# Optimization experiments

Measured on AMD Instinct MI355X. Metric: run time of the kernel, lower is better.

The kernel has to match this reference:

```python
import jax, jax.numpy as jnp
import numpy as np

B, C, H, W = 8, 128, 48, 48
RED = 16  # SELayer reduction


def setup_inputs() -> dict:
    key = jax.random.key(0)
    ks = jax.random.split(key, 8)
    s = 0.05  # weight scale for numerical stability of softmax
    return {
        "x": jax.random.normal(ks[0], (B, C, H, W), jnp.float32),
        "Wq": jax.random.normal(ks[1], (C, C), jnp.float32) * s,
        "bq": jnp.zeros((C,), jnp.float32),
        "Wk": jax.random.normal(ks[2], (C, C), jnp.float32) * s,
        "bk": jnp.zeros((C,), jnp.float32),
        "Wv": jax.random.normal(ks[3], (C, C), jnp.float32) * s,
        "bv": jnp.zeros((C,), jnp.float32),
        "se_w1": jax.random.normal(ks[4], (C // RED, C), jnp.float32) * s,
        "se_w2": jax.random.normal(ks[5], (C, C // RED), jnp.float32) * s,
        "gamma": jax.random.normal(ks[6], (1,), jnp.float32),
    }


def reference(x, Wq, bq, Wk, bk, Wv, bv, se_w1, se_w2, gamma):
    b, c, h, w = x.shape
    n = h * w
    xf = x.reshape(b, c, n)  # (B, C, N)
    # 1x1 convs == per-pixel linear maps over channels
    q = jnp.einsum('oc,bcn->bon', Wq, xf) + bq[None, :, None]  # (B, C, N)
    k = jnp.einsum('oc,bcn->bon', Wk, xf) + bk[None, :, None]
    v = jnp.einsum('oc,bcn->bon', Wv, xf) + bv[None, :, None]
    # energy[b, i, j] = sum_c q[b, c, i] * k[b, c, j]  (unscaled, as in source)
    energy = jnp.einsum('bci,bcj->bij', q, k)  # (B, N, N)
    attn = jax.nn.softmax(energy, axis=-1)
    # out[b, c, i] = sum_j v[b, c, j] * attn[b, i, j]
    out = jnp.einsum('bcj,bij->bci', v, attn).reshape(b, c, h, w)
    # SELayer applied to the input x
    y = jnp.mean(x, axis=(2, 3))  # (B, C) global average pool
    y = jax.nn.relu(y @ se_w1.T)  # (B, C//RED)
    y = jax.nn.sigmoid(y @ se_w2.T)  # (B, C)
    x_se = x * y[:, :, None, None]
    return gamma[0] * out + x_se
```

## Files before the change

kernel.cpp:

```cpp
#include <hip/hip_runtime.h>

typedef _Float16 half8 __attribute__((ext_vector_type(8)));
typedef _Float16 half4 __attribute__((ext_vector_type(4)));
typedef _Float16 half2v __attribute__((ext_vector_type(2)));
typedef float f32x4 __attribute__((ext_vector_type(4)));

#define BATCH 8
#define CH 128
#define NPIX 2304
#define SPLIT 6
#define JPER (NPIX / SPLIT)
#define NT (JPER / 64)
#define BN (BATCH * NPIX)
#define LOG2E 1.44269504088896f

__device__ __forceinline__ f32x4 mfma32(half8 a, half8 b, f32x4 c) {
    return __builtin_amdgcn_mfma_f32_16x16x32_f16(a, b, c, 0, 0, 0);
}
__device__ __forceinline__ f32x4 mfma16(half4 a, half4 b, f32x4 c) {
    return __builtin_amdgcn_mfma_f32_16x16x16f16(a, b, c, 0, 0, 0);
}

__global__ __launch_bounds__(256) void k_prep(
        const float* __restrict__ Wq, const float* __restrict__ Wk,
        const float* __restrict__ Wv, _Float16* __restrict__ Wh) {
    int i = blockIdx.x * 256 + threadIdx.x;
    const float* src = (i < 16384) ? Wq : ((i < 32768) ? Wk : Wv);
    Wh[i] = (_Float16)src[i & 16383];
}

__global__ __launch_bounds__(256) void k_proj(
        const float* __restrict__ x, const _Float16* __restrict__ Wh,
        const float* __restrict__ bq, const float* __restrict__ bk, const float* __restrict__ bv,
        _Float16* __restrict__ qT, _Float16* __restrict__ kT, _Float16* __restrict__ vN,
        float* __restrict__ y0) {
    const int which = blockIdx.z;
    const int t = threadIdx.x;
    const int n0 = blockIdx.x * 128;
    const int b = blockIdx.y;
    const float* bias = (which == 0) ? bq : ((which == 1) ? bk : bv);
    const _Float16* W = Wh + which * 16384;

    __shared__ __align__(16) _Float16 xt[128 * 128];
    __shared__ float ysum[128];

    if (which == 0) {
        if (t < 128) ysum[t] = 0.f;
        __syncthreads();
    }

    {
        const float* xb = x + (size_t)b * CH * NPIX + n0;
        for (int rep = 0; rep < 8; ++rep) {
            int flat = rep * 256 + t;
            int c2 = (flat >> 5) * 2;
            int n4 = (flat & 31) * 4;
            float4 va = *(const float4*)(xb + (size_t)c2 * NPIX + n4);
            float4 vb = *(const float4*)(xb + (size_t)(c2 + 1) * NPIX + n4);
            if (which == 0) {
                atomicAdd(&ysum[c2],     va.x + va.y + va.z + va.w);
                atomicAdd(&ysum[c2 + 1], vb.x + vb.y + vb.z + vb.w);
            }
            int cc = c2 & 7, ck = c2 >> 3;
            *(half2v*)(xt + (n4 + 0) * 128 + ((ck ^ ((n4 + 0) & 7)) * 8) + cc) =
                (half2v){(_Float16)va.x, (_Float16)vb.x};
            *(half2v*)(xt + (n4 + 1) * 128 + ((ck ^ ((n4 + 1) & 7)) * 8) + cc) =
                (half2v){(_Float16)va.y, (_Float16)vb.y};
            *(half2v*)(xt + (n4 + 2) * 128 + ((ck ^ ((n4 + 2) & 7)) * 8) + cc) =
                (half2v){(_Float16)va.z, (_Float16)vb.z};
            *(half2v*)(xt + (n4 + 3) * 128 + ((ck ^ ((n4 + 3) & 7)) * 8) + cc) =
                (half2v){(_Float16)va.w, (_Float16)vb.w};
        }
    }
    __syncthreads();

    if (which == 0 && t < 128)
        atomicAdd(&y0[b * 128 + t], ysum[t]);

    const int lane = t & 63, w = t >> 6;
    const int ln15 = lane & 15, quad = lane >> 4;

    f32x4 zero4 = {0.f, 0.f, 0.f, 0.f};
    f32x4 acc[8][2];
    for (int mt = 0; mt < 8; ++mt) { acc[mt][0] = zero4; acc[mt][1] = zero4; }

    for (int ks = 0; ks < 4; ++ks) {
        half8 bf[2];
        for (int nt = 0; nt < 2; ++nt) {
            int row = w * 32 + nt * 16 + ln15;
            int ch = ks * 4 + quad;
            bf[nt] = *(const half8*)(xt + row * 128 + ((ch ^ (row & 7)) * 8));
        }
        for (int mt = 0; mt < 8; ++mt) {
            half8 af = *(const half8*)(W + (mt * 16 + ln15) * 128 + ks * 32 + quad * 8);
            acc[mt][0] = mfma32(af, bf[0], acc[mt][0]);
            acc[mt][1] = mfma32(af, bf[1], acc[mt][1]);
        }
    }
    __syncthreads();

    if (which == 2) {
        for (int mt = 0; mt < 8; ++mt)
            for (int nt = 0; nt < 2; ++nt)
                for (int r = 0; r < 4; ++r) {
                    int c = mt * 16 + quad * 4 + r;
                    int nl = w * 32 + nt * 16 + ln15;
                    xt[c * 128 + (((nl >> 3) ^ (c & 7)) * 8) + (nl & 7)] =
                        (_Float16)(acc[mt][nt][r] + bias[c]);
                }
        __syncthreads();
        _Float16* vb = vN + (size_t)b * CH * NPIX + n0;
        for (int rep = 0; rep < 8; ++rep) {
            int c = rep * 16 + (t >> 4), ch = t & 15;
            *(half8*)(vb + (size_t)c * NPIX + ch * 8) =
                *(const half8*)(xt + c * 128 + ((ch ^ (c & 7)) * 8));
        }
    } else {
        for (int mt = 0; mt < 8; ++mt)
            for (int nt = 0; nt < 2; ++nt)
                for (int r = 0; r < 4; r += 2) {
                    int c = mt * 16 + quad * 4 + r;
                    int nl = w * 32 + nt * 16 + ln15;
                    *(half2v*)(xt + nl * 128 + (((c >> 3) ^ (nl & 7)) * 8) + (c & 7)) =
                        (half2v){(_Float16)(acc[mt][nt][r] + bias[c]),
                                 (_Float16)(acc[mt][nt][r + 1] + bias[c + 1])};
                }
        __syncthreads();
        _Float16* dst = ((which == 0) ? qT : kT) + ((size_t)b * NPIX + n0) * CH;
        for (int rep = 0; rep < 8; ++rep) {
            int nl = rep * 16 + (t >> 4), ch = t & 15;
            *(half8*)(dst + nl * 128 + ch * 8) =
                *(const half8*)(xt + nl * 128 + ((ch ^ (nl & 7)) * 8));
        }
    }
}

__global__ __launch_bounds__(256, 2) void k_attn(
        const _Float16* __restrict__ qT, const _Float16* __restrict__ kT,
        const _Float16* __restrict__ vN,
        _Float16* __restrict__ o_part, float* __restrict__ g_m, float* __restrict__ g_l) {
    const int i0 = blockIdx.x * 128;
    const int b = blockIdx.y;
    const int split = blockIdx.z;
    const int t = threadIdx.x;
    const int lane = t & 63, w = t >> 6;
    const int ln15 = lane & 15, quad = lane >> 4;

    __shared__ __align__(16) _Float16 sh[16384];
    _Float16* k_s = sh;
    _Float16* v_s = sh + 8192;

    half8 qf[2][4];
    #pragma unroll
    for (int ih = 0; ih < 2; ++ih) {
        const _Float16* qb = qT + ((size_t)b * NPIX + i0 + w * 32 + ih * 16 + ln15) * CH + quad * 8;
        #pragma unroll
        for (int kc = 0; kc < 4; ++kc) qf[ih][kc] = *(const half8*)(qb + kc * 32);
    }

    f32x4 zero4 = {0.f, 0.f, 0.f, 0.f};
    f32x4 os[2][8];
    #pragma unroll
    for (int ih = 0; ih < 2; ++ih)
        for (int ct = 0; ct < 8; ++ct) os[ih][ct] = zero4;
    float m[2] = {-1e30f, -1e30f}, l[2] = {0.f, 0.f};

    for (int it = 0; it < NT; ++it) {
        const int j0 = split * JPER + it * 64;
        __syncthreads();
        {
            const _Float16* kb = kT + ((size_t)b * NPIX + j0) * CH;
            for (int rep = 0; rep < 4; ++rep) {
                int row = rep * 16 + (t >> 4), ch = t & 15;
                *(half8*)(k_s + row * 128 + ((ch ^ (row & 7)) * 8)) =
                    *(const half8*)(kb + row * CH + ch * 8);
            }
        }
        {
            const _Float16* vb = vN + (size_t)b * CH * NPIX + j0;
            for (int rep = 0; rep < 4; ++rep) {
                int c = rep * 32 + (t >> 3), ch = t & 7;
                *(half8*)(v_s + c * 64 + ((ch ^ (c & 7)) * 8)) =
                    *(const half8*)(vb + (size_t)c * NPIX + ch * 8);
            }
        }
        __syncthreads();

        f32x4 s[2][4];
        #pragma unroll
        for (int jt = 0; jt < 4; ++jt) { s[0][jt] = zero4; s[1][jt] = zero4; }
        #pragma unroll
        for (int jt = 0; jt < 4; ++jt) {
            #pragma unroll
            for (int kc = 0; kc < 4; ++kc) {
                int row = jt * 16 + ln15, ch = kc * 4 + quad;
                half8 kf = *(const half8*)(k_s + row * 128 + ((ch ^ (row & 7)) * 8));
                s[0][jt] = mfma32(kf, qf[0][kc], s[0][jt]);
                s[1][jt] = mfma32(kf, qf[1][kc], s[1][jt]);
            }
        }

        half4 pf[2][4];
        #pragma unroll
        for (int ih = 0; ih < 2; ++ih) {
            float mx = fmaxf(fmaxf(s[ih][0][0], s[ih][0][1]), fmaxf(s[ih][0][2], s[ih][0][3]));
            #pragma unroll
            for (int jt = 1; jt < 4; ++jt)
                mx = fmaxf(mx, fmaxf(fmaxf(s[ih][jt][0], s[ih][jt][1]),
                                     fmaxf(s[ih][jt][2], s[ih][jt][3])));
            mx = fmaxf(mx, __shfl_xor(mx, 16));
            mx = fmaxf(mx, __shfl_xor(mx, 32));
            float mnew = fmaxf(m[ih], mx);
            float alpha = exp2f((m[ih] - mnew) * LOG2E);
            m[ih] = mnew;
            float mbias = mnew * LOG2E;

            float sum = 0.f;
            #pragma unroll
            for (int jt = 0; jt < 4; ++jt)
                #pragma unroll
                for (int r = 0; r < 4; ++r) {
                    float p = exp2f(fmaf(s[ih][jt][r], LOG2E, -mbias));
                    sum += p;
                    pf[ih][jt][r] = (_Float16)p;
                }
            sum += __shfl_xor(sum, 16);
            sum += __shfl_xor(sum, 32);
            l[ih] = l[ih] * alpha + sum;

            #pragma unroll
            for (int ct = 0; ct < 8; ++ct) {
                os[ih][ct][0] *= alpha; os[ih][ct][1] *= alpha;
                os[ih][ct][2] *= alpha; os[ih][ct][3] *= alpha;
            }
        }

        #pragma unroll
        for (int ct = 0; ct < 8; ++ct) {
            int c = ct * 16 + ln15;
            #pragma unroll
            for (int jt = 0; jt < 4; ++jt) {
                int chunk = jt * 2 + (quad >> 1);
                half4 vf = *(const half4*)(v_s + c * 64 + ((chunk ^ (c & 7)) * 8) + (quad & 1) * 4);
                os[0][ct] = mfma16(vf, pf[0][jt], os[0][ct]);
                os[1][ct] = mfma16(vf, pf[1][jt], os[1][ct]);
            }
        }
    }

    if (quad == 0) {
        #pragma unroll
        for (int ih = 0; ih < 2; ++ih) {
            int i = i0 + w * 32 + ih * 16 + ln15;
            g_m[(size_t)(split * BATCH + b) * NPIX + i] = m[ih];
            g_l[(size_t)(split * BATCH + b) * NPIX + i] = l[ih];
        }
    }
    __syncthreads();
    #pragma unroll
    for (int ih = 0; ih < 2; ++ih)
        #pragma unroll
        for (int ct = 0; ct < 8; ++ct)
            #pragma unroll
            for (int r = 0; r < 4; ++r) {
                int c = ct * 16 + quad * 4 + r;
                int il = w * 32 + ih * 16 + ln15;
                int chunk = il >> 3;
                sh[c * 128 + ((chunk ^ (c & 7)) * 8) + (il & 7)] = (_Float16)os[ih][ct][r];
            }
    __syncthreads();
    _Float16* op = o_part + (size_t)(split * BATCH + b) * CH * NPIX;
    for (int rep = 0; rep < 8; ++rep) {
        int c = rep * 16 + (t >> 4), ch = t & 15;
        *(half8*)(op + (size_t)c * NPIX + i0 + ch * 8) =
            *(const half8*)(sh + c * 128 + ((ch ^ (c & 7)) * 8));
    }
}

__global__ __launch_bounds__(256) void k_combine(
        const _Float16* __restrict__ o_part, const float* __restrict__ g_m,
        const float* __restrict__ g_l, const float* __restrict__ x,
        const float* __restrict__ y0, const float* __restrict__ se_w1,
        const float* __restrict__ se_w2, const float* __restrict__ gamma_p,
        float* __restrict__ out) {
    const int i0 = blockIdx.x * 64;
    const int b = blockIdx.y;
    const int t = threadIdx.x;
    __shared__ float wl[SPLIT][64];
    __shared__ float ly[128];
    __shared__ float ly1[8];
    __shared__ float scs[32];

    if (t < 128) ly[t] = y0[b * 128 + t] * (1.0f / (float)NPIX);
    if (t < 64) {
        int i = i0 + t;
        float mm[SPLIT], llv[SPLIT];
        float M = -1e30f;
        for (int s = 0; s < SPLIT; ++s) {
            mm[s] = g_m[(size_t)(s * BATCH + b) * NPIX + i];
            llv[s] = g_l[(size_t)(s * BATCH + b) * NPIX + i];
            M = fmaxf(M, mm[s]);
        }
        float L = 0.f, e[SPLIT];
        for (int s = 0; s < SPLIT; ++s) {
            e[s] = exp2f((mm[s] - M) * LOG2E);
            L += e[s] * llv[s];
        }
        float inv = 1.f / L;
        for (int s = 0; s < SPLIT; ++s) wl[s][t] = e[s] * inv;
    }
    __syncthreads();
    if (t < 8) {
        float a = 0.f;
        for (int c = 0; c < 128; ++c) a += se_w1[t * 128 + c] * ly[c];
        ly1[t] = fmaxf(a, 0.f);
    }
    __syncthreads();
    if (t < 32) {
        int c = blockIdx.z * 32 + t;
        float a = 0.f;
        for (int r = 0; r < 8; ++r) a += se_w2[c * 8 + r] * ly1[r];
        scs[t] = 1.f / (1.f + __expf(-a));
    }
    __syncthreads();

    const float g = gamma_p[0];
    {
        int c = blockIdx.z * 32 + (t >> 3), i8 = (t & 7) * 8;
        size_t base = ((size_t)b * CH + c) * NPIX + i0 + i8;
        float acc[8] = {0.f, 0.f, 0.f, 0.f, 0.f, 0.f, 0.f, 0.f};
        for (int s = 0; s < SPLIT; ++s) {
            half8 o = *(const half8*)(o_part +
                ((size_t)(s * BATCH + b) * CH + c) * NPIX + i0 + i8);
            for (int e = 0; e < 8; ++e) acc[e] += wl[s][i8 + e] * (float)o[e];
        }
        float sc = scs[t >> 3];
        float4 x0 = *(const float4*)(x + base);
        float4 x1 = *(const float4*)(x + base + 4);
        float4 r0, r1;
        r0.x = g * acc[0] + x0.x * sc; r0.y = g * acc[1] + x0.y * sc;
        r0.z = g * acc[2] + x0.z * sc; r0.w = g * acc[3] + x0.w * sc;
        r1.x = g * acc[4] + x1.x * sc; r1.y = g * acc[5] + x1.y * sc;
        r1.z = g * acc[6] + x1.z * sc; r1.w = g * acc[7] + x1.w * sc;
        *(float4*)(out + base) = r0;
        *(float4*)(out + base + 4) = r1;
    }
}

extern "C" void kernel_launch(void* const* d_in, const int* in_sizes, int n_in,
                              void* d_out, int out_size, void* d_ws, size_t ws_size,
                              hipStream_t stream) {
    const float* x     = (const float*)d_in[0];
    const float* Wq    = (const float*)d_in[1];
    const float* bq    = (const float*)d_in[2];
    const float* Wk    = (const float*)d_in[3];
    const float* bk    = (const float*)d_in[4];
    const float* Wv    = (const float*)d_in[5];
    const float* bv    = (const float*)d_in[6];
    const float* se_w1 = (const float*)d_in[7];
    const float* se_w2 = (const float*)d_in[8];
    const float* gamma = (const float*)d_in[9];
    float* out = (float*)d_out;

    char* ws = (char*)d_ws;
    const size_t E = (size_t)BATCH * NPIX * CH;
    _Float16* qT = (_Float16*)(ws);
    _Float16* kT = (_Float16*)(ws + E * 2);
    _Float16* vN = (_Float16*)(ws + E * 4);
    _Float16* op = (_Float16*)(ws + E * 6);
    char* tail   = ws + E * 6 + (size_t)SPLIT * E * 2;
    _Float16* Wh = (_Float16*)(tail);
    float* g_m   = (float*)(tail + 98304);
    float* g_l   = (float*)(tail + 98304 + (size_t)SPLIT * BN * 4);
    float* y0    = (float*)(tail + 98304 + 2 * (size_t)SPLIT * BN * 4);

    hipMemsetAsync(y0, 0, 1024 * sizeof(float), stream);
    k_prep<<<192, 256, 0, stream>>>(Wq, Wk, Wv, Wh);
    k_proj<<<dim3(NPIX / 128, BATCH, 3), 256, 0, stream>>>(
        x, Wh, bq, bk, bv, qT, kT, vN, y0);
    k_attn<<<dim3(NPIX / 128, BATCH, SPLIT), 256, 0, stream>>>(
        qT, kT, vN, op, g_m, g_l);
    k_combine<<<dim3(NPIX / 64, BATCH, 4), 256, 0, stream>>>(
        op, g_m, g_l, x, y0, se_w1, se_w2, gamma, out);
}
```

Measured before the change: 159.0 us.

## Enlarge attention query tile to 192 rows and replace SE atomics with partial sums

The attention kernel now processes 192 query rows per block as three 64-row groups per wave, so each K/V tile loaded into shared memory is reused across more queries. The block count falls from 864 to 576 and the launch bound no longer requests two blocks per SM. This raises register pressure and may reduce occupancy. The SE global pooling now writes per-tile partial sums that the combine kernel reduces, removing the global atomic and the memset launch.

```diff
diff --git a/kernel.cpp b/kernel.cpp
--- a/kernel.cpp
+++ b/kernel.cpp
@@ -8,6 +8,9 @@
 #define BATCH 8
 #define CH 128
 #define NPIX 2304
+#define NTILE 18
+#define NGRP 3
+#define ITILE 192
 #define SPLIT 6
 #define JPER (NPIX / SPLIT)
 #define NT (JPER / 64)
@@ -33,7 +36,7 @@
         const float* __restrict__ x, const _Float16* __restrict__ Wh,
         const float* __restrict__ bq, const float* __restrict__ bk, const float* __restrict__ bv,
         _Float16* __restrict__ qT, _Float16* __restrict__ kT, _Float16* __restrict__ vN,
-        float* __restrict__ y0) {
+        float* __restrict__ y0p) {
     const int which = blockIdx.z;
     const int t = threadIdx.x;
     const int n0 = blockIdx.x * 128;
@@ -75,7 +78,7 @@
     __syncthreads();
 
     if (which == 0 && t < 128)
-        atomicAdd(&y0[b * 128 + t], ysum[t]);
+        y0p[((size_t)blockIdx.x * BATCH + b) * 128 + t] = ysum[t];
 
     const int lane = t & 63, w = t >> 6;
     const int ln15 = lane & 15, quad = lane >> 4;
@@ -135,11 +138,11 @@
     }
 }
 
-__global__ __launch_bounds__(256, 2) void k_attn(
+__global__ __launch_bounds__(256) void k_attn(
         const _Float16* __restrict__ qT, const _Float16* __restrict__ kT,
         const _Float16* __restrict__ vN,
         _Float16* __restrict__ o_part, float* __restrict__ g_m, float* __restrict__ g_l) {
-    const int i0 = blockIdx.x * 128;
+    const int i0 = blockIdx.x * ITILE;
     const int b = blockIdx.y;
     const int split = blockIdx.z;
     const int t = threadIdx.x;
@@ -150,20 +153,22 @@
     _Float16* k_s = sh;
     _Float16* v_s = sh + 8192;
 
-    half8 qf[2][4];
+    half8 qf[NGRP][4];
     #pragma unroll
-    for (int ih = 0; ih < 2; ++ih) {
-        const _Float16* qb = qT + ((size_t)b * NPIX + i0 + w * 32 + ih * 16 + ln15) * CH + quad * 8;
+    for (int ih = 0; ih < NGRP; ++ih) {
+        const _Float16* qb = qT + ((size_t)b * NPIX + i0 + ih * 64 + w * 16 + ln15) * CH + quad * 8;
         #pragma unroll
         for (int kc = 0; kc < 4; ++kc) qf[ih][kc] = *(const half8*)(qb + kc * 32);
     }
 
     f32x4 zero4 = {0.f, 0.f, 0.f, 0.f};
-    f32x4 os[2][8];
+    f32x4 os[NGRP][8];
     #pragma unroll
-    for (int ih = 0; ih < 2; ++ih)
+    for (int ih = 0; ih < NGRP; ++ih)
         for (int ct = 0; ct < 8; ++ct) os[ih][ct] = zero4;
-    float m[2] = {-1e30f, -1e30f}, l[2] = {0.f, 0.f};
+    float m[NGRP], l[NGRP];
+    #pragma unroll
+    for (int ih = 0; ih < NGRP; ++ih) { m[ih] = -1e30f; l[ih] = 0.f; }
 
     for (int it = 0; it < NT; ++it) {
         const int j0 = split * JPER + it * 64;
@@ -186,23 +191,26 @@
         }
         __syncthreads();
 
-        f32x4 s[2][4];
-        #pragma unroll
-        for (int jt = 0; jt < 4; ++jt) { s[0][jt] = zero4; s[1][jt] = zero4; }
+        f32x4 s[NGRP][4];
+        #pragma unroll
+        for (int ih = 0; ih < NGRP; ++ih)
+            #pragma unroll
+            for (int jt = 0; jt < 4; ++jt) s[ih][jt] = zero4;
         #pragma unroll
         for (int jt = 0; jt < 4; ++jt) {
             #pragma unroll
             for (int kc = 0; kc < 4; ++kc) {
                 int row = jt * 16 + ln15, ch = kc * 4 + quad;
                 half8 kf = *(const half8*)(k_s + row * 128 + ((ch ^ (row & 7)) * 8));
-                s[0][jt] = mfma32(kf, qf[0][kc], s[0][jt]);
-                s[1][jt] = mfma32(kf, qf[1][kc], s[1][jt]);
-            }
-        }
-
-        half4 pf[2][4];
-        #pragma unroll
-        for (int ih = 0; ih < 2; ++ih) {
+                #pragma unroll
+                for (int ih = 0; ih < NGRP; ++ih)
+                    s[ih][jt] = mfma32(kf, qf[ih][kc], s[ih][jt]);
+            }
+        }
+
+        half4 pf[NGRP][4];
+        #pragma unroll
+        for (int ih = 0; ih < NGRP; ++ih) {
             float mx = fmaxf(fmaxf(s[ih][0][0], s[ih][0][1]), fmaxf(s[ih][0][2], s[ih][0][3]));
             #pragma unroll
             for (int jt = 1; jt < 4; ++jt)
@@ -242,45 +250,47 @@
             for (int jt = 0; jt < 4; ++jt) {
                 int chunk = jt * 2 + (quad >> 1);
                 half4 vf = *(const half4*)(v_s + c * 64 + ((chunk ^ (c & 7)) * 8) + (quad & 1) * 4);
-                os[0][ct] = mfma16(vf, pf[0][jt], os[0][ct]);
-                os[1][ct] = mfma16(vf, pf[1][jt], os[1][ct]);
+                #pragma unroll
+                for (int ih = 0; ih < NGRP; ++ih)
+                    os[ih][ct] = mfma16(vf, pf[ih][jt], os[ih][ct]);
             }
         }
     }
 
     if (quad == 0) {
         #pragma unroll
-        for (int ih = 0; ih < 2; ++ih) {
-            int i = i0 + w * 32 + ih * 16 + ln15;
+        for (int ih = 0; ih < NGRP; ++ih) {
+            int i = i0 + ih * 64 + w * 16 + ln15;
             g_m[(size_t)(split * BATCH + b) * NPIX + i] = m[ih];
             g_l[(size_t)(split * BATCH + b) * NPIX + i] = l[ih];
         }
     }
-    __syncthreads();
+    _Float16* op = o_part + (size_t)(split * BATCH + b) * CH * NPIX;
     #pragma unroll
-    for (int ih = 0; ih < 2; ++ih)
+    for (int ih = 0; ih < NGRP; ++ih) {
+        __syncthreads();
         #pragma unroll
         for (int ct = 0; ct < 8; ++ct)
             #pragma unroll
             for (int r = 0; r < 4; ++r) {
                 int c = ct * 16 + quad * 4 + r;
-                int il = w * 32 + ih * 16 + ln15;
+                int il = w * 16 + ln15;
                 int chunk = il >> 3;
-                sh[c * 128 + ((chunk ^ (c & 7)) * 8) + (il & 7)] = (_Float16)os[ih][ct][r];
-            }
-    __syncthreads();
-    _Float16* op = o_part + (size_t)(split * BATCH + b) * CH * NPIX;
-    for (int rep = 0; rep < 8; ++rep) {
-        int c = rep * 16 + (t >> 4), ch = t & 15;
-        *(half8*)(op + (size_t)c * NPIX + i0 + ch * 8) =
-            *(const half8*)(sh + c * 128 + ((ch ^ (c & 7)) * 8));
+                sh[c * 64 + ((chunk ^ (c & 7)) * 8) + (il & 7)] = (_Float16)os[ih][ct][r];
+            }
+        __syncthreads();
+        for (int rep = 0; rep < 4; ++rep) {
+            int c = rep * 32 + (t >> 3), ch = t & 7;
+            *(half8*)(op + (size_t)c * NPIX + i0 + ih * 64 + ch * 8) =
+                *(const half8*)(sh + c * 64 + ((ch ^ (c & 7)) * 8));
+        }
     }
 }
 
 __global__ __launch_bounds__(256) void k_combine(
         const _Float16* __restrict__ o_part, const float* __restrict__ g_m,
         const float* __restrict__ g_l, const float* __restrict__ x,
-        const float* __restrict__ y0, const float* __restrict__ se_w1,
+        const float* __restrict__ y0p, const float* __restrict__ se_w1,
         const float* __restrict__ se_w2, const float* __restrict__ gamma_p,
         float* __restrict__ out) {
     const int i0 = blockIdx.x * 64;
@@ -291,7 +301,12 @@
     __shared__ float ly1[8];
     __shared__ float scs[32];
 
-    if (t < 128) ly[t] = y0[b * 128 + t] * (1.0f / (float)NPIX);
+    if (t < 128) {
+        float a = 0.f;
+        for (int tl = 0; tl < NTILE; ++tl)
+            a += y0p[((size_t)tl * BATCH + b) * 128 + t];
+        ly[t] = a * (1.0f / (float)NPIX);
+    }
     if (t < 64) {
         int i = i0 + t;
         float mm[SPLIT], llv[SPLIT];
@@ -372,14 +387,13 @@
     _Float16* Wh = (_Float16*)(tail);
     float* g_m   = (float*)(tail + 98304);
     float* g_l   = (float*)(tail + 98304 + (size_t)SPLIT * BN * 4);
-    float* y0    = (float*)(tail + 98304 + 2 * (size_t)SPLIT * BN * 4);
-
-    hipMemsetAsync(y0, 0, 1024 * sizeof(float), stream);
+    float* y0p   = (float*)(tail + 98304 + 2 * (size_t)SPLIT * BN * 4);
+
     k_prep<<<192, 256, 0, stream>>>(Wq, Wk, Wv, Wh);
-    k_proj<<<dim3(NPIX / 128, BATCH, 3), 256, 0, stream>>>(
-        x, Wh, bq, bk, bv, qT, kT, vN, y0);
-    k_attn<<<dim3(NPIX / 128, BATCH, SPLIT), 256, 0, stream>>>(
+    k_proj<<<dim3(NTILE, BATCH, 3), 256, 0, stream>>>(
+        x, Wh, bq, bk, bv, qT, kT, vN, y0p);
+    k_attn<<<dim3(NPIX / ITILE, BATCH, SPLIT), 256, 0, stream>>>(
         qT, kT, vN, op, g_m, g_l);
     k_combine<<<dim3(NPIX / 64, BATCH, 4), 256, 0, stream>>>(
-        op, g_m, g_l, x, y0, se_w1, se_w2, gamma, out);
-}
+        op, g_m, g_l, x, y0p, se_w1, se_w2, gamma, out);
+}
```

Result: slower. 185.8 us (+16.8%).
